# Optimization experiments

Hardware: AMD Instinct MI355X
Metric: run time of the kernel (lower is better)

The kernel has to match this reference:

```python
import jax, jax.numpy as jnp
import numpy as np

# Problem dims
N_LIG, N_PROT = 10000, 40000
N = N_LIG + N_PROT            # total nodes in batched graph
E = 400000                    # total edges (avg degree 8)
B = 512                       # number of pocket graphs in batch
F_LIG, F_PROT = 74, 1280      # ligand / protein node feature dims
H, D = 4, 64                  # GAT heads, per-head dim
HD = H * D                    # hidden size == PROJ_DIM == 256


def setup_inputs() -> dict:
    key = jax.random.key(0)
    ks = jax.random.split(key, 16)
    s = jnp.float32(0.05)  # keep activations tame
    return {
        "ligand_x":  jax.random.normal(ks[0], (N_LIG, F_LIG), jnp.float32),
        "protein_x": jax.random.normal(ks[1], (N_PROT, F_PROT), jnp.float32),
        "W_lig":  jax.random.normal(ks[2], (F_LIG, HD), jnp.float32) * s,
        "W_prot": jax.random.normal(ks[3], (F_PROT, HD), jnp.float32) * s,
        "W1":     jax.random.normal(ks[4], (HD, HD), jnp.float32) * s,
        "a1_src": jax.random.normal(ks[5], (H, D), jnp.float32) * s,
        "a1_dst": jax.random.normal(ks[6], (H, D), jnp.float32) * s,
        "W2":     jax.random.normal(ks[7], (HD, HD), jnp.float32) * s,
        "a2_src": jax.random.normal(ks[8], (H, D), jnp.float32) * s,
        "a2_dst": jax.random.normal(ks[9], (H, D), jnp.float32) * s,
        "W_out":  jax.random.normal(ks[10], (HD + 1, 1), jnp.float32) * s,
        "b_out":  jnp.zeros((1,), jnp.float32),
        "edge_src":  jax.random.randint(ks[11], (E,), 0, N, jnp.int32),
        "edge_dst":  jax.random.randint(ks[12], (E,), 0, N, jnp.int32),
        "graph_ids": jnp.sort(jax.random.randint(ks[13], (N,), 0, B, jnp.int32)),
        "scores":    jax.random.uniform(ks[14], (B, 1), jnp.float32),
    }


def _gat_layer(x, W, a_src, a_dst, src, dst):
    """Multi-head GAT layer over an edge list. x:[N,HD] -> [N,HD]."""
    n = x.shape[0]
    h = (x @ W).reshape(n, H, D)                               # [N,H,D]
    att_s = jnp.einsum('nhd,hd->nh', h, a_src)                 # [N,H]
    att_d = jnp.einsum('nhd,hd->nh', h, a_dst)
    e = jax.nn.leaky_relu(att_s[src] + att_d[dst], 0.2)        # [E,H]
    # edge softmax over incoming edges of each destination node
    m = jax.ops.segment_max(e, dst, num_segments=n)            # [N,H]
    w = jnp.exp(e - m[dst])                                    # [E,H]
    denom = jax.ops.segment_sum(w, dst, num_segments=n)        # [N,H]
    agg = jax.ops.segment_sum(h[src] * w[..., None], dst, num_segments=n)  # [N,H,D]
    out = agg / (denom[..., None] + 1e-9)
    return jax.nn.elu(out).reshape(n, HD)


def reference(ligand_x, protein_x, W_lig, W_prot, W1, a1_src, a1_dst,
              W2, a2_src, a2_dst, W_out, b_out,
              edge_src, edge_dst, graph_ids, scores):
    # per-node-type input projection into shared hidden space
    x = jnp.concatenate([ligand_x @ W_lig, protein_x @ W_prot], axis=0)  # [N,HD]
    h = _gat_layer(x, W1, a1_src, a1_dst, edge_src, edge_dst)
    h = _gat_layer(h, W2, a2_src, a2_dst, edge_src, edge_dst)
    # mean pooling per graph -> [B, PROJ_DIM]
    gsum = jax.ops.segment_sum(h, graph_ids, num_segments=B)
    cnt = jax.ops.segment_sum(jnp.ones((h.shape[0], 1), h.dtype), graph_ids, num_segments=B)
    pooled = gsum / jnp.maximum(cnt, 1.0)
    # concat docking score, final linear (dropout is identity at eval)
    feat = jnp.concatenate([pooled, scores], axis=1)           # [B, PROJ_DIM+1]
    return feat @ W_out + b_out                                 # [B,1]
```

## Files before the change

kernel.cpp:

```cpp
#include <hip/hip_runtime.h>
#include <hip/hip_bf16.h>

#define N_LIG   10000
#define N_PROT  40000
#define NN      50000
#define EDGES   400000
#define BATCH   512
#define F_LIG   74
#define F_PROT  1280
#define HD      256
#define HEADS   4
#define DIM     64

typedef __bf16 bf16x8 __attribute__((ext_vector_type(8)));
typedef __bf16 bf16x4 __attribute__((ext_vector_type(4)));
typedef float  f32x4  __attribute__((ext_vector_type(4)));


__global__ void k_hist(const int* __restrict__ dst, int* __restrict__ counts, int E) {
    int e = blockIdx.x * blockDim.x + threadIdx.x;
    if (e < E) atomicAdd(&counts[dst[e]], 1);
}

__global__ __launch_bounds__(1024) void k_scan1(const int* __restrict__ counts,
                                                int* __restrict__ incl,
                                                int* __restrict__ bsum, int N) {
    __shared__ int tmp[1024];
    int i = blockIdx.x * 1024 + threadIdx.x;
    int v = (i < N) ? counts[i] : 0;
    tmp[threadIdx.x] = v;
    __syncthreads();
    for (int off = 1; off < 1024; off <<= 1) {
        int add = (threadIdx.x >= (unsigned)off) ? tmp[threadIdx.x - off] : 0;
        __syncthreads();
        tmp[threadIdx.x] += add;
        __syncthreads();
    }
    if (i < N) incl[i] = tmp[threadIdx.x];
    if (threadIdx.x == 1023) bsum[blockIdx.x] = tmp[1023];
}

__global__ void k_scan2(int* __restrict__ bsum, int nb, int* __restrict__ row_ptr, int N, int E) {
    if (threadIdx.x == 0 && blockIdx.x == 0) {
        int run = 0;
        for (int i = 0; i < nb; ++i) { int v = bsum[i]; bsum[i] = run; run += v; }
        row_ptr[N] = E;
    }
}

__global__ __launch_bounds__(1024) void k_scan3(const int* __restrict__ incl,
                                                const int* __restrict__ counts,
                                                const int* __restrict__ bsum,
                                                int* __restrict__ row_ptr, int N) {
    int i = blockIdx.x * 1024 + threadIdx.x;
    if (i < N) row_ptr[i] = bsum[blockIdx.x] + incl[i] - counts[i];
}

__global__ void k_scatter(const int* __restrict__ src, const int* __restrict__ dst,
                          const int* __restrict__ row_ptr, int* __restrict__ cursor,
                          int* __restrict__ csr_src, int E) {
    int e = blockIdx.x * blockDim.x + threadIdx.x;
    if (e < E) {
        int d = dst[e];
        int pos = row_ptr[d] + atomicAdd(&cursor[d], 1);
        csr_src[pos] = src[e];
    }
}

__global__ __launch_bounds__(256) void k_wcvt(const float* __restrict__ W,
                                              __bf16* __restrict__ Bt, int K, int Kp) {
    int n = blockIdx.x;
    for (int k = threadIdx.x; k < Kp; k += blockDim.x)
        Bt[(size_t)n * Kp + k] = (k < K) ? (__bf16)W[(size_t)k * HD + n] : (__bf16)0.f;
}

template <int MODE>
__global__ __launch_bounds__(256, MODE ? 4 : 5)
void mfma_gemm(const float* __restrict__ A, const __bf16* __restrict__ Bt,
               float* __restrict__ C,
               __bf16* __restrict__ Hbf, float* __restrict__ atts, float* __restrict__ attd,
               const float* __restrict__ a_src, const float* __restrict__ a_dst,
               int M, int K, int Kp) {
    __shared__ __align__(16) unsigned char smem[MODE ? (18432 + 20480) : (10240 + 20480)];
    __bf16* sAh = (__bf16*)smem;
    float*  sAf = (float*)smem;
    __bf16* sB  = (__bf16*)(smem + (MODE ? 18432 : 10240));

    int tid  = threadIdx.x;
    int bm   = blockIdx.y * 64;
    int bn   = blockIdx.x * 128;
    int lane = tid & 63, wave = tid >> 6;
    int wr   = wave >> 1, wc = wave & 1;
    int l15  = lane & 15, quad = lane >> 4;

    f32x4 acc[2][4];
    #pragma unroll
    for (int i = 0; i < 2; ++i)
        #pragma unroll
        for (int j = 0; j < 4; ++j)
            acc[i][j] = (f32x4){0.f, 0.f, 0.f, 0.f};

    const bool k4 = (K & 3) == 0;
    float  va[2][4];
    bf16x8 vb[2];

    auto loadTile = [&](int k0) {
        bool fullk = k4 && (k0 + 32 <= K);
        #pragma unroll
        for (int it = 0; it < 2; ++it) {
            int fl = tid + it * 256, row = fl >> 3, kq = fl & 7;
            int gm = bm + row;
            if (gm < M && fullk) {
                f32x4 t = *(const f32x4*)&A[(size_t)gm * K + k0 + kq * 4];
                va[it][0] = t[0]; va[it][1] = t[1]; va[it][2] = t[2]; va[it][3] = t[3];
            } else {
                #pragma unroll
                for (int j = 0; j < 4; ++j) {
                    int gk = k0 + kq * 4 + j;
                    va[it][j] = (gm < M && gk < K) ? A[(size_t)gm * K + gk] : 0.f;
                }
            }
        }
        #pragma unroll
        for (int it = 0; it < 2; ++it) {
            int fl = tid + it * 256, n = fl >> 2, seg = fl & 3;
            vb[it] = *(const bf16x8*)&Bt[(size_t)(bn + n) * Kp + k0 + seg * 8];
        }
    };
    auto storeTile = [&](int buf) {
        #pragma unroll
        for (int it = 0; it < 2; ++it) {
            int fl = tid + it * 256, row = fl >> 3, kq = fl & 7;
            if (MODE == 0) {
                bf16x4 hi;
                #pragma unroll
                for (int j = 0; j < 4; ++j) hi[j] = (__bf16)va[it][j];
                *(bf16x4*)&sAh[buf * 2560 + row * 40 + kq * 4] = hi;
            } else {
                f32x4 t = {va[it][0], va[it][1], va[it][2], va[it][3]};
                *(f32x4*)&sAf[buf * 2304 + row * 36 + kq * 4] = t;
            }
        }
        #pragma unroll
        for (int it = 0; it < 2; ++it) {
            int fl = tid + it * 256, n = fl >> 2, seg = fl & 3;
            *(bf16x8*)&sB[buf * 5120 + n * 40 + seg * 8] = vb[it];
        }
    };

    int nsteps = (K + 31) / 32;
    loadTile(0);
    storeTile(0);

    for (int s = 0; s < nsteps; ++s) {
        bool more = (s + 1) < nsteps;
        if (more) loadTile((s + 1) * 32);
        __syncthreads();
        int cur = s & 1;

        bf16x8 af[2], al[2], bfr[4];
        #pragma unroll
        for (int i = 0; i < 2; ++i) {
            if (MODE == 0) {
                af[i] = *(bf16x8*)&sAh[cur * 2560 + (wr * 32 + i * 16 + l15) * 40 + quad * 8];
            } else {
                int base = cur * 2304 + (wr * 32 + i * 16 + l15) * 36 + quad * 8;
                f32x4 p0 = *(f32x4*)&sAf[base];
                f32x4 p1 = *(f32x4*)&sAf[base + 4];
                #pragma unroll
                for (int c = 0; c < 8; ++c) {
                    float x = (c < 4) ? p0[c] : p1[c - 4];
                    __bf16 h = (__bf16)x;
                    af[i][c] = h;
                    al[i][c] = (__bf16)(x - (float)h);
                }
            }
        }
        #pragma unroll
        for (int j = 0; j < 4; ++j)
            bfr[j] = *(bf16x8*)&sB[cur * 5120 + (wc * 64 + j * 16 + l15) * 40 + quad * 8];

        #pragma unroll
        for (int i = 0; i < 2; ++i)
            #pragma unroll
            for (int j = 0; j < 4; ++j) {
                acc[i][j] = __builtin_amdgcn_mfma_f32_16x16x32_bf16(af[i], bfr[j], acc[i][j], 0, 0, 0);
                if (MODE)
                    acc[i][j] = __builtin_amdgcn_mfma_f32_16x16x32_bf16(al[i], bfr[j], acc[i][j], 0, 0, 0);
            }
        if (more) storeTile(cur ^ 1);
    }

    if (MODE == 0) {
        #pragma unroll
        for (int i = 0; i < 2; ++i)
            #pragma unroll
            for (int r = 0; r < 4; ++r) {
                int m = bm + wr * 32 + i * 16 + quad * 4 + r;
                if (m < M) {
                    #pragma unroll
                    for (int j = 0; j < 4; ++j)
                        C[(size_t)m * HD + bn + wc * 64 + j * 16 + l15] = acc[i][j][r];
                }
            }
    } else {
        int head = (bn >> 6) + wc;
        float as[4], ad2[4];
        #pragma unroll
        for (int j = 0; j < 4; ++j) {
            as[j]  = a_src[head * DIM + j * 16 + l15];
            ad2[j] = a_dst[head * DIM + j * 16 + l15];
        }
        #pragma unroll
        for (int i = 0; i < 2; ++i)
            #pragma unroll
            for (int r = 0; r < 4; ++r) {
                int m = bm + wr * 32 + i * 16 + quad * 4 + r;
                bool ok = m < M;
                float s = 0.f, t = 0.f;
                #pragma unroll
                for (int j = 0; j < 4; ++j) {
                    float v = acc[i][j][r];
                    if (ok) Hbf[(size_t)m * HD + head * DIM + j * 16 + l15] = (__bf16)v;
                    s += v * as[j];
                    t += v * ad2[j];
                }
                #pragma unroll
                for (int mask = 1; mask <= 8; mask <<= 1) {
                    s += __shfl_xor(s, mask, 64);
                    t += __shfl_xor(t, mask, 64);
                }
                if (ok && l15 == 0) {
                    atts[m * HEADS + head] = s;
                    attd[m * HEADS + head] = t;
                }
            }
    }
}

__global__ __launch_bounds__(256) void gat_agg(const __bf16* __restrict__ hW,
                                               const float* __restrict__ att_s,
                                               const float* __restrict__ att_d,
                                               const int* __restrict__ row_ptr,
                                               const int* __restrict__ csr_src,
                                               float* __restrict__ out, int N) {
    int n = blockIdx.x;
    int t = threadIdx.x;
    int lane = t & 63, head = t >> 6;
    int r0 = row_ptr[n], deg = row_ptr[n + 1] - r0;
    float ad = att_d[n * HEADS + head];

    float m = -INFINITY;
    for (int base = 0; base < deg; base += 64) {
        int i = base + lane;
        float e = -INFINITY;
        if (i < deg) {
            int s = csr_src[r0 + i];
            float x = att_s[s * HEADS + head] + ad;
            e = (x >= 0.f) ? x : 0.2f * x;
        }
        for (int off = 32; off > 0; off >>= 1) e = fmaxf(e, __shfl_xor(e, off, 64));
        m = fmaxf(m, e);
    }

    f32x4 acc4 = (f32x4){0.f, 0.f, 0.f, 0.f};
    float wsum = 0.f;
    int sub = lane >> 4;
    int dq  = lane & 15;
    for (int base = 0; base < deg; base += 64) {
        int i = base + lane;
        float w = 0.f; int s = 0;
        if (i < deg) {
            s = csr_src[r0 + i];
            float x = att_s[s * HEADS + head] + ad;
            x = (x >= 0.f) ? x : 0.2f * x;
            w = expf(x - m);
        }
        wsum += w;
        int cnt = min(64, deg - base);
        for (int j0 = 0; j0 < cnt; j0 += 8) {
            #pragma unroll
            for (int g = 0; g < 2; ++g) {
                int e0 = j0 + g * 4 + sub;
                int ec = min(e0, cnt - 1);
                int   sj = __shfl(s, ec, 64);
                float wj = __shfl(w, ec, 64);
                if (e0 >= cnt) wj = 0.f;
                bf16x4 v4 = *(const bf16x4*)&hW[(size_t)sj * HD + head * DIM + dq * 4];
                #pragma unroll
                for (int c = 0; c < 4; ++c) acc4[c] += wj * (float)v4[c];
            }
        }
    }
    #pragma unroll
    for (int c = 0; c < 4; ++c) {
        acc4[c] += __shfl_xor(acc4[c], 16, 64);
        acc4[c] += __shfl_xor(acc4[c], 32, 64);
    }
    for (int off = 32; off > 0; off >>= 1) wsum += __shfl_xor(wsum, off, 64);
    if (sub == 0) {
        float inv = 1.f / (wsum + 1e-9f);
        f32x4 o;
        #pragma unroll
        for (int c = 0; c < 4; ++c) {
            float v = acc4[c] * inv;
            o[c] = (v > 0.f) ? v : expm1f(v);
        }
        *(f32x4*)&out[(size_t)n * HD + head * DIM + dq * 4] = o;
    }
}

__global__ __launch_bounds__(256) void pool_out(const float* __restrict__ h,
                                                const int* __restrict__ gid,
                                                const float* __restrict__ W_out,
                                                const float* __restrict__ b_out,
                                                const float* __restrict__ scores,
                                                float* __restrict__ out, int N) {
    int b = blockIdx.x;
    int j = threadIdx.x;
    int l = 0, r = N;
    while (l < r) { int mid = (l + r) >> 1; if (gid[mid] < b) l = mid + 1; else r = mid; }
    int lo = l;
    r = N;
    while (l < r) { int mid = (l + r) >> 1; if (gid[mid] < b + 1) l = mid + 1; else r = mid; }
    int hi = l;

    float sum = 0.f;
    for (int n = lo; n < hi; ++n) sum += h[(size_t)n * HD + j];
    int cnt = hi - lo;
    float pooled = sum / fmaxf((float)cnt, 1.f);
    float val = pooled * W_out[j];

    __shared__ float red[256];
    red[j] = val;
    __syncthreads();
    for (int s = 128; s > 0; s >>= 1) {
        if (j < s) red[j] += red[j + s];
        __syncthreads();
    }
    if (j == 0) {
        out[b] = red[0] + scores[b] * W_out[HD] + b_out[0];
    }
}


static inline size_t al256(size_t x) { return (x + 255) & ~(size_t)255; }

#define KP_LIG  96
#define KP_PROT 1280
#define KP_HID  256

extern "C" void kernel_launch(void* const* d_in, const int* in_sizes, int n_in,
                              void* d_out, int out_size, void* d_ws, size_t ws_size,
                              hipStream_t stream) {
    const float* ligand_x  = (const float*)d_in[0];
    const float* protein_x = (const float*)d_in[1];
    const float* W_lig     = (const float*)d_in[2];
    const float* W_prot    = (const float*)d_in[3];
    const float* W1        = (const float*)d_in[4];
    const float* a1_src    = (const float*)d_in[5];
    const float* a1_dst    = (const float*)d_in[6];
    const float* W2        = (const float*)d_in[7];
    const float* a2_src    = (const float*)d_in[8];
    const float* a2_dst    = (const float*)d_in[9];
    const float* W_out     = (const float*)d_in[10];
    const float* b_out     = (const float*)d_in[11];
    const int*   edge_src  = (const int*)d_in[12];
    const int*   edge_dst  = (const int*)d_in[13];
    const int*   graph_ids = (const int*)d_in[14];
    const float* scores    = (const float*)d_in[15];
    float* out = (float*)d_out;

    char* w = (char*)d_ws;
    float*  xbuf = (float*)w;           w += al256((size_t)NN * HD * 4);
    __bf16* Hbf  = (__bf16*)w;          w += al256((size_t)NN * HD * 2);
    float* atts = (float*)w;            w += al256((size_t)NN * HEADS * 4);
    float* attd = (float*)w;            w += al256((size_t)NN * HEADS * 4);
    int* counts  = (int*)w;             w += al256((size_t)NN * 4);
    int* incl    = (int*)w;             w += al256((size_t)NN * 4);
    int* bsum    = (int*)w;             w += al256(64 * 4);
    int* row_ptr = (int*)w;             w += al256((size_t)(NN + 1) * 4);
    int* cursor  = (int*)w;             w += al256((size_t)NN * 4);
    int* csr_src = (int*)w;             w += al256((size_t)EDGES * 4);
    __bf16* Bt_lig  = (__bf16*)w;       w += al256((size_t)HD * KP_LIG * 2);
    __bf16* Bt_prot = (__bf16*)w;       w += al256((size_t)HD * KP_PROT * 2);
    __bf16* Bt_W1   = (__bf16*)w;       w += al256((size_t)HD * KP_HID * 2);
    __bf16* Bt_W2   = (__bf16*)w;       w += al256((size_t)HD * KP_HID * 2);

    const int NB_SCAN = (NN + 1023) / 1024;

    hipMemsetAsync(counts, 0, (size_t)NN * 4, stream);
    hipMemsetAsync(cursor, 0, (size_t)NN * 4, stream);

    k_wcvt<<<HD, 256, 0, stream>>>(W_lig,  Bt_lig,  F_LIG,  KP_LIG);
    k_wcvt<<<HD, 256, 0, stream>>>(W_prot, Bt_prot, F_PROT, KP_PROT);
    k_wcvt<<<HD, 256, 0, stream>>>(W1,     Bt_W1,   HD,     KP_HID);
    k_wcvt<<<HD, 256, 0, stream>>>(W2,     Bt_W2,   HD,     KP_HID);

    k_hist<<<(EDGES + 255) / 256, 256, 0, stream>>>(edge_dst, counts, EDGES);
    k_scan1<<<NB_SCAN, 1024, 0, stream>>>(counts, incl, bsum, NN);
    k_scan2<<<1, 1, 0, stream>>>(bsum, NB_SCAN, row_ptr, NN, EDGES);
    k_scan3<<<NB_SCAN, 1024, 0, stream>>>(incl, counts, bsum, row_ptr, NN);
    k_scatter<<<(EDGES + 255) / 256, 256, 0, stream>>>(edge_src, edge_dst, row_ptr,
                                                       cursor, csr_src, EDGES);

    mfma_gemm<0><<<dim3(2, (N_LIG + 63) / 64), 256, 0, stream>>>(
        ligand_x, Bt_lig, xbuf, nullptr, nullptr, nullptr, nullptr, nullptr,
        N_LIG, F_LIG, KP_LIG);
    mfma_gemm<0><<<dim3(2, (N_PROT + 63) / 64), 256, 0, stream>>>(
        protein_x, Bt_prot, xbuf + (size_t)N_LIG * HD, nullptr, nullptr, nullptr,
        nullptr, nullptr, N_PROT, F_PROT, KP_PROT);

    mfma_gemm<1><<<dim3(2, (NN + 63) / 64), 256, 0, stream>>>(
        xbuf, Bt_W1, nullptr, Hbf, atts, attd, a1_src, a1_dst, NN, HD, KP_HID);
    gat_agg<<<NN, 256, 0, stream>>>(Hbf, atts, attd, row_ptr, csr_src, xbuf, NN);

    mfma_gemm<1><<<dim3(2, (NN + 63) / 64), 256, 0, stream>>>(
        xbuf, Bt_W2, nullptr, Hbf, atts, attd, a2_src, a2_dst, NN, HD, KP_HID);
    gat_agg<<<NN, 256, 0, stream>>>(Hbf, atts, attd, row_ptr, csr_src, xbuf, NN);

    pool_out<<<BATCH, 256, 0, stream>>>(xbuf, graph_ids, W_out, b_out, scores, out, NN);
}
```

Before: 741.9 us.

## Load GEMM operands directly from global into MFMA fragments, dropping LDS staging

The MFMA GEMM no longer stages A and B tiles through double-buffered shared memory with block barriers. Each lane now loads its own fragment straight from global memory, prefetching the next A step into registers, and launch bounds are unified to 4 blocks. This removes LDS traffic and __syncthreads, but loses reuse across waves: each B element is reloaded by both row-waves and each A element by both column-waves. Loads become strided per-lane accesses, less coalesced than before.

```diff
diff --git a/kernel.cpp b/kernel.cpp
--- a/kernel.cpp
+++ b/kernel.cpp
@@ -75,17 +75,12 @@
 }
 
 template <int MODE>
-__global__ __launch_bounds__(256, MODE ? 4 : 5)
+__global__ __launch_bounds__(256, 4)
 void mfma_gemm(const float* __restrict__ A, const __bf16* __restrict__ Bt,
                float* __restrict__ C,
                __bf16* __restrict__ Hbf, float* __restrict__ atts, float* __restrict__ attd,
                const float* __restrict__ a_src, const float* __restrict__ a_dst,
                int M, int K, int Kp) {
-    __shared__ __align__(16) unsigned char smem[MODE ? (18432 + 20480) : (10240 + 20480)];
-    __bf16* sAh = (__bf16*)smem;
-    float*  sAf = (float*)smem;
-    __bf16* sB  = (__bf16*)(smem + (MODE ? 18432 : 10240));
-
     int tid  = threadIdx.x;
     int bm   = blockIdx.y * 64;
     int bn   = blockIdx.x * 128;
@@ -100,85 +95,65 @@
         for (int j = 0; j < 4; ++j)
             acc[i][j] = (f32x4){0.f, 0.f, 0.f, 0.f};
 
-    const bool k4 = (K & 3) == 0;
-    float  va[2][4];
-    bf16x8 vb[2];
-
-    auto loadTile = [&](int k0) {
-        bool fullk = k4 && (k0 + 32 <= K);
-        #pragma unroll
-        for (int it = 0; it < 2; ++it) {
-            int fl = tid + it * 256, row = fl >> 3, kq = fl & 7;
-            int gm = bm + row;
-            if (gm < M && fullk) {
-                f32x4 t = *(const f32x4*)&A[(size_t)gm * K + k0 + kq * 4];
-                va[it][0] = t[0]; va[it][1] = t[1]; va[it][2] = t[2]; va[it][3] = t[3];
+    bool rokA[2];
+    const float* pA[2];
+    #pragma unroll
+    for (int i = 0; i < 2; ++i) {
+        int r = bm + wr * 32 + i * 16 + l15;
+        rokA[i] = r < M;
+        pA[i] = A + (size_t)(rokA[i] ? r : 0) * K + quad * 8;
+    }
+    const __bf16* pB[4];
+    #pragma unroll
+    for (int j = 0; j < 4; ++j)
+        pB[j] = Bt + (size_t)(bn + wc * 64 + j * 16 + l15) * Kp + quad * 8;
+
+    int nsteps = (K + 31) / 32;
+
+    f32x4 a0[2], a1[2];
+    f32x4 n0[2], n1[2];
+
+    auto loadA = [&](int k0, f32x4 (&x0)[2], f32x4 (&x1)[2]) {
+        bool fullk = (k0 + 32) <= K;
+        #pragma unroll
+        for (int i = 0; i < 2; ++i) {
+            if (fullk && rokA[i]) {
+                x0[i] = *(const f32x4*)(pA[i] + k0);
+                x1[i] = *(const f32x4*)(pA[i] + k0 + 4);
             } else {
                 #pragma unroll
-                for (int j = 0; j < 4; ++j) {
-                    int gk = k0 + kq * 4 + j;
-                    va[it][j] = (gm < M && gk < K) ? A[(size_t)gm * K + gk] : 0.f;
+                for (int c = 0; c < 4; ++c) {
+                    int kbase = k0 + quad * 8 + c;
+                    x0[i][c] = (rokA[i] && kbase     < K) ? pA[i][k0 + c]     : 0.f;
+                    x1[i][c] = (rokA[i] && kbase + 4 < K) ? pA[i][k0 + 4 + c] : 0.f;
                 }
             }
         }
-        #pragma unroll
-        for (int it = 0; it < 2; ++it) {
-            int fl = tid + it * 256, n = fl >> 2, seg = fl & 3;
-            vb[it] = *(const bf16x8*)&Bt[(size_t)(bn + n) * Kp + k0 + seg * 8];
-        }
     };
-    auto storeTile = [&](int buf) {
-        #pragma unroll
-        for (int it = 0; it < 2; ++it) {
-            int fl = tid + it * 256, row = fl >> 3, kq = fl & 7;
-            if (MODE == 0) {
-                bf16x4 hi;
-                #pragma unroll
-                for (int j = 0; j < 4; ++j) hi[j] = (__bf16)va[it][j];
-                *(bf16x4*)&sAh[buf * 2560 + row * 40 + kq * 4] = hi;
-            } else {
-                f32x4 t = {va[it][0], va[it][1], va[it][2], va[it][3]};
-                *(f32x4*)&sAf[buf * 2304 + row * 36 + kq * 4] = t;
-            }
-        }
-        #pragma unroll
-        for (int it = 0; it < 2; ++it) {
-            int fl = tid + it * 256, n = fl >> 2, seg = fl & 3;
-            *(bf16x8*)&sB[buf * 5120 + n * 40 + seg * 8] = vb[it];
-        }
-    };
-
-    int nsteps = (K + 31) / 32;
-    loadTile(0);
-    storeTile(0);
+
+    loadA(0, a0, a1);
 
     for (int s = 0; s < nsteps; ++s) {
         bool more = (s + 1) < nsteps;
-        if (more) loadTile((s + 1) * 32);
-        __syncthreads();
-        int cur = s & 1;
-
-        bf16x8 af[2], al[2], bfr[4];
+        if (more) loadA((s + 1) * 32, n0, n1);
+
+        int k0 = s * 32;
+        bf16x8 bfr[4];
+        #pragma unroll
+        for (int j = 0; j < 4; ++j)
+            bfr[j] = *(const bf16x8*)(pB[j] + k0);
+
+        bf16x8 af[2], al[2];
         #pragma unroll
         for (int i = 0; i < 2; ++i) {
-            if (MODE == 0) {
-                af[i] = *(bf16x8*)&sAh[cur * 2560 + (wr * 32 + i * 16 + l15) * 40 + quad * 8];
-            } else {
-                int base = cur * 2304 + (wr * 32 + i * 16 + l15) * 36 + quad * 8;
-                f32x4 p0 = *(f32x4*)&sAf[base];
-                f32x4 p1 = *(f32x4*)&sAf[base + 4];
-                #pragma unroll
-                for (int c = 0; c < 8; ++c) {
-                    float x = (c < 4) ? p0[c] : p1[c - 4];
-                    __bf16 h = (__bf16)x;
-                    af[i][c] = h;
-                    al[i][c] = (__bf16)(x - (float)h);
-                }
-            }
-        }
-        #pragma unroll
-        for (int j = 0; j < 4; ++j)
-            bfr[j] = *(bf16x8*)&sB[cur * 5120 + (wc * 64 + j * 16 + l15) * 40 + quad * 8];
+            #pragma unroll
+            for (int c = 0; c < 8; ++c) {
+                float x = (c < 4) ? a0[i][c] : a1[i][c - 4];
+                __bf16 h = (__bf16)x;
+                af[i][c] = h;
+                if (MODE) al[i][c] = (__bf16)(x - (float)h);
+            }
+        }
 
         #pragma unroll
         for (int i = 0; i < 2; ++i)
@@ -188,7 +163,9 @@
                 if (MODE)
                     acc[i][j] = __builtin_amdgcn_mfma_f32_16x16x32_bf16(al[i], bfr[j], acc[i][j], 0, 0, 0);
             }
-        if (more) storeTile(cur ^ 1);
+
+        #pragma unroll
+        for (int i = 0; i < 2; ++i) { a0[i] = n0[i]; a1[i] = n1[i]; }
     }
 
     if (MODE == 0) {
```

New measurement: 883.3 us. +19.1%, slower.
